# Kernel optimization log

Hardware: AMD Instinct MI355X
Metric: run time of the kernel (lower is better)

Reference implementation:

```python
import jax, jax.numpy as jnp
import numpy as np
import math

PHI = (1 + math.sqrt(5)) / 2
VOCAB = 50257
EMBED_DIM = 1024
NUM_WINDINGS = 8
EPS = 1e-5


def _generate_coprimes(n):
    coprimes = [1, 2]
    while len(coprimes) < n:
        nxt = int(coprimes[-1] * PHI) + 1
        while any(math.gcd(nxt, c) > 1 for c in coprimes):
            nxt += 1
        coprimes.append(nxt)
    return coprimes[:n]


def setup_inputs() -> dict:
    key = jax.random.key(0)
    k1, k2, k3 = jax.random.split(key, 3)
    B, S = 8, 4096
    x = jax.random.randint(k1, (B, S), 0, VOCAB, dtype=jnp.int64)
    windings = jnp.asarray(_generate_coprimes(NUM_WINDINGS), dtype=jnp.float32)
    win_dim = 2 * NUM_WINDINGS
    # nn.Linear default init: U(-1/sqrt(fan_in), 1/sqrt(fan_in))
    bound = 1.0 / math.sqrt(win_dim)
    proj_w = jax.random.uniform(k2, (EMBED_DIM, win_dim), jnp.float32, -bound, bound)
    proj_b = jax.random.uniform(k3, (EMBED_DIM,), jnp.float32, -bound, bound)
    gamma = jnp.ones((EMBED_DIM,), jnp.float32)
    beta = jnp.zeros((EMBED_DIM,), jnp.float32)
    return {"x": x, "windings": windings, "proj_w": proj_w, "proj_b": proj_b,
            "gamma": gamma, "beta": beta}


def reference(x, windings, proj_w, proj_b, gamma, beta):
    # t in [0,1): fractional position on the torus
    t = x.astype(jnp.float32) / VOCAB                      # (B, S)
    angle = (2.0 * jnp.pi) * t[..., None] * windings       # (B, S, W)
    # torch loop appends cos, sin per winding -> interleaved [cos0,sin0,cos1,sin1,...]
    feats = jnp.stack([jnp.cos(angle), jnp.sin(angle)], axis=-1)  # (B, S, W, 2)
    feats = feats.reshape(*angle.shape[:-1], 2 * windings.shape[0])  # (B, S, 2W)
    emb = jnp.einsum('bsf,df->bsd', feats, proj_w) + proj_b  # (B, S, D)
    # SyntonicNorm: LayerNorm-style normalization over embed_dim with affine params
    mu = jnp.mean(emb, axis=-1, keepdims=True)
    var = jnp.mean(jnp.square(emb - mu), axis=-1, keepdims=True)
    normed = (emb - mu) * jax.lax.rsqrt(var + EPS)
    return normed * gamma + beta
```

## Files before the change

kernel.cpp:

```cpp
#include <hip/hip_runtime.h>
#include <math.h>


#define TWO_PI 6.28318530717958647692f
#define INV_VOCAB (1.0f / 50257.0f)
#define INV_D (1.0f / 1024.0f)

__global__ __launch_bounds__(256) void wind_fused(const int* __restrict__ x,
                                                  const float* __restrict__ winds,
                                                  const float* __restrict__ pw,
                                                  const float* __restrict__ pb,
                                                  const float* __restrict__ gamma,
                                                  const float* __restrict__ beta,
                                                  float* __restrict__ out) {
  __shared__ __align__(16) float feat[16][20];
  __shared__ float red[2][4][8][2];

  const int tid = threadIdx.x;
  const int wave = tid >> 6;
  const int lane = tid & 63;
  const int base = blockIdx.x * 16;
  const int d0 = tid << 2;

  float4 wreg[4][4];
#pragma unroll
  for (int r = 0; r < 4; ++r)
#pragma unroll
    for (int c = 0; c < 4; ++c)
      wreg[r][c] = reinterpret_cast<const float4*>(pw)[(d0 + r) * 4 + c];
  const float4 pbv = reinterpret_cast<const float4*>(pb)[tid];
  const float4 gv = reinterpret_cast<const float4*>(gamma)[tid];
  const float4 bv = reinterpret_cast<const float4*>(beta)[tid];

  {
    const int rl = tid >> 4;
    const int j = tid & 15;
    const float tf = (float)x[base + rl] * INV_VOCAB;
    float s, c;
    sincosf(TWO_PI * tf * winds[j >> 1], &s, &c);
    feat[rl][j] = (j & 1) ? s : c;
  }
  __syncthreads();

#pragma unroll
  for (int h = 0; h < 2; ++h) {
    float er[8][4];
    float sr[8], qr[8];

#pragma unroll
    for (int r = 0; r < 8; ++r) {
      const int rr = h * 8 + r;
      const float4 F0 = *reinterpret_cast<const float4*>(&feat[rr][0]);
      const float4 F1 = *reinterpret_cast<const float4*>(&feat[rr][4]);
      const float4 F2 = *reinterpret_cast<const float4*>(&feat[rr][8]);
      const float4 F3 = *reinterpret_cast<const float4*>(&feat[rr][12]);
#pragma unroll
      for (int k = 0; k < 4; ++k) {
        float a = (k == 0) ? pbv.x : (k == 1) ? pbv.y : (k == 2) ? pbv.z : pbv.w;
        a = fmaf(wreg[k][0].x, F0.x, a);
        a = fmaf(wreg[k][0].y, F0.y, a);
        a = fmaf(wreg[k][0].z, F0.z, a);
        a = fmaf(wreg[k][0].w, F0.w, a);
        a = fmaf(wreg[k][1].x, F1.x, a);
        a = fmaf(wreg[k][1].y, F1.y, a);
        a = fmaf(wreg[k][1].z, F1.z, a);
        a = fmaf(wreg[k][1].w, F1.w, a);
        a = fmaf(wreg[k][2].x, F2.x, a);
        a = fmaf(wreg[k][2].y, F2.y, a);
        a = fmaf(wreg[k][2].z, F2.z, a);
        a = fmaf(wreg[k][2].w, F2.w, a);
        a = fmaf(wreg[k][3].x, F3.x, a);
        a = fmaf(wreg[k][3].y, F3.y, a);
        a = fmaf(wreg[k][3].z, F3.z, a);
        a = fmaf(wreg[k][3].w, F3.w, a);
        er[r][k] = a;
      }
      sr[r] = (er[r][0] + er[r][1]) + (er[r][2] + er[r][3]);
      float q = er[r][0] * er[r][0];
      q = fmaf(er[r][1], er[r][1], q);
      q = fmaf(er[r][2], er[r][2], q);
      q = fmaf(er[r][3], er[r][3], q);
      qr[r] = q;
    }

#pragma unroll
    for (int r = 0; r < 8; ++r) {
#pragma unroll
      for (int off = 1; off < 64; off <<= 1) {
        sr[r] += __shfl_xor(sr[r], off);
        qr[r] += __shfl_xor(qr[r], off);
      }
    }
    if (lane == 0) {
#pragma unroll
      for (int r = 0; r < 8; ++r) {
        red[h][wave][r][0] = sr[r];
        red[h][wave][r][1] = qr[r];
      }
    }
    __syncthreads();

    float* o = out + (size_t)(base + h * 8) * 1024 + d0;
#pragma unroll
    for (int r = 0; r < 8; ++r) {
      const float s = (red[h][0][r][0] + red[h][1][r][0]) +
                      (red[h][2][r][0] + red[h][3][r][0]);
      const float q = (red[h][0][r][1] + red[h][1][r][1]) +
                      (red[h][2][r][1] + red[h][3][r][1]);
      const float mu = s * INV_D;
      const float var = fmaf(q, INV_D, -mu * mu);
      const float rs = rsqrtf(var + 1e-5f);
      const float s0 = gv.x * rs, s1 = gv.y * rs, s2 = gv.z * rs, s3 = gv.w * rs;
      float4 res;
      res.x = fmaf(er[r][0], s0, fmaf(-mu, s0, bv.x));
      res.y = fmaf(er[r][1], s1, fmaf(-mu, s1, bv.y));
      res.z = fmaf(er[r][2], s2, fmaf(-mu, s2, bv.z));
      res.w = fmaf(er[r][3], s3, fmaf(-mu, s3, bv.w));
      *reinterpret_cast<float4*>(o + (size_t)r * 1024) = res;
    }
  }
}

extern "C" void kernel_launch(void* const* d_in, const int* in_sizes, int n_in,
                              void* d_out, int out_size, void* d_ws, size_t ws_size,
                              hipStream_t stream) {
  const int* x = (const int*)d_in[0];
  const float* winds = (const float*)d_in[1];
  const float* pw = (const float*)d_in[2];
  const float* pb = (const float*)d_in[3];
  const float* gamma = (const float*)d_in[4];
  const float* beta = (const float*)d_in[5];
  float* out = (float*)d_out;

  const int rows = in_sizes[0];
  wind_fused<<<rows / 16, 256, 0, stream>>>(x, winds, pw, pb, gamma, beta, out);
}
```

Before: 45.78 us.

## Precompute weight Gram statistics to get LayerNorm moments without full-row reductions

Adds a one-block pre-kernel that computes the Gram matrix W^T W, column sums, weight-bias cross terms and bias moments, all scaled by 1/D. The main kernel derives each row's mean and variance from these 16x16 statistics and the features, so it no longer needs cross-wave reductions over 1024 outputs. Each block now covers 256 output columns for 32 rows on a 2D grid, and the embedding is recomputed in a streaming write loop. The cost is an extra serial kernel launch. Computing variance as E[x^2]-mu^2 from the expanded form can lose precision.

```diff
diff --git a/kernel.cpp b/kernel.cpp
--- a/kernel.cpp
+++ b/kernel.cpp
@@ -5,119 +5,155 @@
 #define TWO_PI 6.28318530717958647692f
 #define INV_VOCAB (1.0f / 50257.0f)
 #define INV_D (1.0f / 1024.0f)
+#define ROWS_PB 32
 
-__global__ __launch_bounds__(256) void wind_fused(const int* __restrict__ x,
-                                                  const float* __restrict__ winds,
-                                                  const float* __restrict__ pw,
+typedef float f32x4 __attribute__((ext_vector_type(4)));
+
+__global__ __launch_bounds__(256) void wind_stats(const float* __restrict__ pw,
                                                   const float* __restrict__ pb,
-                                                  const float* __restrict__ gamma,
-                                                  const float* __restrict__ beta,
-                                                  float* __restrict__ out) {
-  __shared__ __align__(16) float feat[16][20];
-  __shared__ float red[2][4][8][2];
+                                                  float* __restrict__ ws) {
+  __shared__ __align__(16) float wtile[64][16];
+  __shared__ float btile[64];
+  const int t = threadIdx.x;
+  const int j = t >> 4, i = t & 15;
+
+  float m = 0.f, mw = 0.f, cc = 0.f, b1 = 0.f, b2 = 0.f;
+  for (int tile = 0; tile < 16; ++tile) {
+    *reinterpret_cast<f32x4*>(&wtile[0][0] + t * 4) =
+        *reinterpret_cast<const f32x4*>(pw + tile * 1024 + t * 4);
+    if (t < 64) btile[t] = pb[tile * 64 + t];
+    __syncthreads();
+#pragma unroll 8
+    for (int dd = 0; dd < 64; ++dd) {
+      const float wj = wtile[dd][j];
+      const float wi = wtile[dd][i];
+      m = fmaf(wj, wi, m);
+      if (i == 0) {
+        const float bb = btile[dd];
+        mw += wj;
+        cc = fmaf(wj, bb, cc);
+        if (j == 0) {
+          b1 += bb;
+          b2 = fmaf(bb, bb, b2);
+        }
+      }
+    }
+    __syncthreads();
+  }
+  ws[t] = m * INV_D;
+  if (i == 0) {
+    ws[256 + j] = mw * INV_D;
+    ws[272 + j] = cc * INV_D;
+    if (j == 0) {
+      ws[288] = b1 * INV_D;
+      ws[289] = b2 * INV_D;
+    }
+  }
+}
+
+__global__ __launch_bounds__(256) void wind_main(const int* __restrict__ x,
+                                                 const float* __restrict__ winds,
+                                                 const float* __restrict__ pw,
+                                                 const float* __restrict__ pb,
+                                                 const float* __restrict__ gamma,
+                                                 const float* __restrict__ beta,
+                                                 const float* __restrict__ ws,
+                                                 float* __restrict__ out) {
+  __shared__ __align__(16) float feat[ROWS_PB][20];
+  __shared__ __align__(16) float Mlds[16][20];
+  __shared__ float mwl[16], cl[16], cst[2];
+  __shared__ float murs[ROWS_PB][2];
 
   const int tid = threadIdx.x;
-  const int wave = tid >> 6;
-  const int lane = tid & 63;
-  const int base = blockIdx.x * 16;
-  const int d0 = tid << 2;
+  const int d = blockIdx.x * 256 + tid;
+  const int row0 = blockIdx.y * ROWS_PB;
 
-  float4 wreg[4][4];
+  Mlds[tid >> 4][tid & 15] = ws[tid];
+  if (tid < 16) mwl[tid] = ws[256 + tid];
+  else if (tid < 32) cl[tid - 16] = ws[272 + tid - 16];
+  else if (tid < 34) cst[tid - 32] = ws[288 + tid - 32];
+
+  const f32x4 w0 = reinterpret_cast<const f32x4*>(pw)[d * 4 + 0];
+  const f32x4 w1 = reinterpret_cast<const f32x4*>(pw)[d * 4 + 1];
+  const f32x4 w2 = reinterpret_cast<const f32x4*>(pw)[d * 4 + 2];
+  const f32x4 w3 = reinterpret_cast<const f32x4*>(pw)[d * 4 + 3];
+  const float pbd = pb[d];
+  const float gd = gamma[d];
+  const float bd = beta[d];
+
 #pragma unroll
-  for (int r = 0; r < 4; ++r)
-#pragma unroll
-    for (int c = 0; c < 4; ++c)
-      wreg[r][c] = reinterpret_cast<const float4*>(pw)[(d0 + r) * 4 + c];
-  const float4 pbv = reinterpret_cast<const float4*>(pb)[tid];
-  const float4 gv = reinterpret_cast<const float4*>(gamma)[tid];
-  const float4 bv = reinterpret_cast<const float4*>(beta)[tid];
-
-  {
-    const int rl = tid >> 4;
-    const int j = tid & 15;
-    const float tf = (float)x[base + rl] * INV_VOCAB;
-    float s, c;
-    sincosf(TWO_PI * tf * winds[j >> 1], &s, &c);
-    feat[rl][j] = (j & 1) ? s : c;
+  for (int s = 0; s < 2; ++s) {
+    const int slot = tid + s * 256;
+    const int r = slot >> 4, jj = slot & 15;
+    const float tf = (float)x[row0 + r] * INV_VOCAB;
+    float sn, cs;
+    sincosf(TWO_PI * tf * winds[jj >> 1], &sn, &cs);
+    feat[r][jj] = (jj & 1) ? sn : cs;
   }
   __syncthreads();
 
+  {
+    const int jj = tid & 15;
+    const float mwj = mwl[jj];
+    const float cj = cl[jj];
+    const f32x4 M0 = *reinterpret_cast<const f32x4*>(&Mlds[jj][0]);
+    const f32x4 M1 = *reinterpret_cast<const f32x4*>(&Mlds[jj][4]);
+    const f32x4 M2 = *reinterpret_cast<const f32x4*>(&Mlds[jj][8]);
+    const f32x4 M3 = *reinterpret_cast<const f32x4*>(&Mlds[jj][12]);
 #pragma unroll
-  for (int h = 0; h < 2; ++h) {
-    float er[8][4];
-    float sr[8], qr[8];
-
+    for (int h = 0; h < 2; ++h) {
+      const int r = (tid >> 4) + h * 16;
+      const f32x4 F0 = *reinterpret_cast<const f32x4*>(&feat[r][0]);
+      const f32x4 F1 = *reinterpret_cast<const f32x4*>(&feat[r][4]);
+      const f32x4 F2 = *reinterpret_cast<const f32x4*>(&feat[r][8]);
+      const f32x4 F3 = *reinterpret_cast<const f32x4*>(&feat[r][12]);
+      float acc = 0.f;
+      acc = fmaf(M0.x, F0.x, acc); acc = fmaf(M0.y, F0.y, acc);
+      acc = fmaf(M0.z, F0.z, acc); acc = fmaf(M0.w, F0.w, acc);
+      acc = fmaf(M1.x, F1.x, acc); acc = fmaf(M1.y, F1.y, acc);
+      acc = fmaf(M1.z, F1.z, acc); acc = fmaf(M1.w, F1.w, acc);
+      acc = fmaf(M2.x, F2.x, acc); acc = fmaf(M2.y, F2.y, acc);
+      acc = fmaf(M2.z, F2.z, acc); acc = fmaf(M2.w, F2.w, acc);
+      acc = fmaf(M3.x, F3.x, acc); acc = fmaf(M3.y, F3.y, acc);
+      acc = fmaf(M3.z, F3.z, acc); acc = fmaf(M3.w, F3.w, acc);
+      const float fjj = feat[r][jj];
+      float pE = fjj * fmaf(2.f, cj, acc);
+      float pM = fjj * mwj;
 #pragma unroll
-    for (int r = 0; r < 8; ++r) {
-      const int rr = h * 8 + r;
-      const float4 F0 = *reinterpret_cast<const float4*>(&feat[rr][0]);
-      const float4 F1 = *reinterpret_cast<const float4*>(&feat[rr][4]);
-      const float4 F2 = *reinterpret_cast<const float4*>(&feat[rr][8]);
-      const float4 F3 = *reinterpret_cast<const float4*>(&feat[rr][12]);
-#pragma unroll
-      for (int k = 0; k < 4; ++k) {
-        float a = (k == 0) ? pbv.x : (k == 1) ? pbv.y : (k == 2) ? pbv.z : pbv.w;
-        a = fmaf(wreg[k][0].x, F0.x, a);
-        a = fmaf(wreg[k][0].y, F0.y, a);
-        a = fmaf(wreg[k][0].z, F0.z, a);
-        a = fmaf(wreg[k][0].w, F0.w, a);
-        a = fmaf(wreg[k][1].x, F1.x, a);
-        a = fmaf(wreg[k][1].y, F1.y, a);
-        a = fmaf(wreg[k][1].z, F1.z, a);
-        a = fmaf(wreg[k][1].w, F1.w, a);
-        a = fmaf(wreg[k][2].x, F2.x, a);
-        a = fmaf(wreg[k][2].y, F2.y, a);
-        a = fmaf(wreg[k][2].z, F2.z, a);
-        a = fmaf(wreg[k][2].w, F2.w, a);
-        a = fmaf(wreg[k][3].x, F3.x, a);
-        a = fmaf(wreg[k][3].y, F3.y, a);
-        a = fmaf(wreg[k][3].z, F3.z, a);
-        a = fmaf(wreg[k][3].w, F3.w, a);
-        er[r][k] = a;
+      for (int off = 1; off < 16; off <<= 1) {
+        pE += __shfl_xor(pE, off);
+        pM += __shfl_xor(pM, off);
       }
-      sr[r] = (er[r][0] + er[r][1]) + (er[r][2] + er[r][3]);
-      float q = er[r][0] * er[r][0];
-      q = fmaf(er[r][1], er[r][1], q);
-      q = fmaf(er[r][2], er[r][2], q);
-      q = fmaf(er[r][3], er[r][3], q);
-      qr[r] = q;
-    }
-
-#pragma unroll
-    for (int r = 0; r < 8; ++r) {
-#pragma unroll
-      for (int off = 1; off < 64; off <<= 1) {
-        sr[r] += __shfl_xor(sr[r], off);
-        qr[r] += __shfl_xor(qr[r], off);
+      if (jj == 0) {
+        const float mu = pM + cst[0];
+        const float var = (pE + cst[1]) - mu * mu;
+        murs[r][0] = mu;
+        murs[r][1] = rsqrtf(var + 1e-5f);
       }
     }
-    if (lane == 0) {
-#pragma unroll
-      for (int r = 0; r < 8; ++r) {
-        red[h][wave][r][0] = sr[r];
-        red[h][wave][r][1] = qr[r];
-      }
-    }
-    __syncthreads();
+  }
+  __syncthreads();
 
-    float* o = out + (size_t)(base + h * 8) * 1024 + d0;
-#pragma unroll
-    for (int r = 0; r < 8; ++r) {
-      const float s = (red[h][0][r][0] + red[h][1][r][0]) +
-                      (red[h][2][r][0] + red[h][3][r][0]);
-      const float q = (red[h][0][r][1] + red[h][1][r][1]) +
-                      (red[h][2][r][1] + red[h][3][r][1]);
-      const float mu = s * INV_D;
-      const float var = fmaf(q, INV_D, -mu * mu);
-      const float rs = rsqrtf(var + 1e-5f);
-      const float s0 = gv.x * rs, s1 = gv.y * rs, s2 = gv.z * rs, s3 = gv.w * rs;
-      float4 res;
-      res.x = fmaf(er[r][0], s0, fmaf(-mu, s0, bv.x));
-      res.y = fmaf(er[r][1], s1, fmaf(-mu, s1, bv.y));
-      res.z = fmaf(er[r][2], s2, fmaf(-mu, s2, bv.z));
-      res.w = fmaf(er[r][3], s3, fmaf(-mu, s3, bv.w));
-      *reinterpret_cast<float4*>(o + (size_t)r * 1024) = res;
-    }
+  float* o = out + (size_t)row0 * 1024 + d;
+#pragma unroll 2
+  for (int r = 0; r < ROWS_PB; ++r) {
+    const f32x4 F0 = *reinterpret_cast<const f32x4*>(&feat[r][0]);
+    const f32x4 F1 = *reinterpret_cast<const f32x4*>(&feat[r][4]);
+    const f32x4 F2 = *reinterpret_cast<const f32x4*>(&feat[r][8]);
+    const f32x4 F3 = *reinterpret_cast<const f32x4*>(&feat[r][12]);
+    float e = pbd;
+    e = fmaf(w0.x, F0.x, e); e = fmaf(w0.y, F0.y, e);
+    e = fmaf(w0.z, F0.z, e); e = fmaf(w0.w, F0.w, e);
+    e = fmaf(w1.x, F1.x, e); e = fmaf(w1.y, F1.y, e);
+    e = fmaf(w1.z, F1.z, e); e = fmaf(w1.w, F1.w, e);
+    e = fmaf(w2.x, F2.x, e); e = fmaf(w2.y, F2.y, e);
+    e = fmaf(w2.z, F2.z, e); e = fmaf(w2.w, F2.w, e);
+    e = fmaf(w3.x, F3.x, e); e = fmaf(w3.y, F3.y, e);
+    e = fmaf(w3.z, F3.z, e); e = fmaf(w3.w, F3.w, e);
+    const float mu = murs[r][0];
+    const float rs = murs[r][1];
+    const float a = rs * gd;
+    o[(size_t)r * 1024] = fmaf(e, a, fmaf(-mu, a, bd));
   }
 }
 
@@ -131,7 +167,10 @@
   const float* gamma = (const float*)d_in[4];
   const float* beta = (const float*)d_in[5];
   float* out = (float*)d_out;
+  float* ws = (float*)d_ws;
 
   const int rows = in_sizes[0];
-  wind_fused<<<rows / 16, 256, 0, stream>>>(x, winds, pw, pb, gamma, beta, out);
+  wind_stats<<<1, 256, 0, stream>>>(pw, pb, ws);
+  dim3 grid(4, (unsigned)(rows / ROWS_PB));
+  wind_main<<<grid, 256, 0, stream>>>(x, winds, pw, pb, gamma, beta, ws, out);
 }
```

Result: slower. 112.9 us (+146.6%).
